# Performance work log

Hardware: AMD Instinct MI355X
Metric: run time of the kernel (lower is better)

## Reference

```python
import jax, jax.numpy as jnp
import numpy as np

HIDDEN = 1024
B, S = 4, 2048

def setup_inputs() -> dict:
    key = jax.random.key(0)
    ks = jax.random.split(key, 8)
    scale = 1.0 / np.sqrt(HIDDEN)
    return {
        "x": jax.random.normal(ks[0], (B, S, HIDDEN), dtype=jnp.float32),
        "mask": jax.random.randint(ks[1], (B, S, S), 0, 2, dtype=jnp.int32),
        "Wq": jax.random.normal(ks[2], (HIDDEN, HIDDEN), dtype=jnp.float32) * scale,
        "bq": jax.random.normal(ks[3], (HIDDEN,), dtype=jnp.float32) * 0.01,
        "Wk": jax.random.normal(ks[4], (HIDDEN, HIDDEN), dtype=jnp.float32) * scale,
        "bk": jax.random.normal(ks[5], (HIDDEN,), dtype=jnp.float32) * 0.01,
        "Wv": jax.random.normal(ks[6], (HIDDEN, HIDDEN), dtype=jnp.float32) * scale,
        "bv": jax.random.normal(ks[7], (HIDDEN,), dtype=jnp.float32) * 0.01,
    }

def reference(x, mask, Wq, bq, Wk, bk, Wv, bv):
    # torch Linear: y = x @ W.T + b
    Q = jnp.einsum("bsh,oh->bso", x, Wq) + bq
    K = jnp.einsum("bsh,oh->bso", x, Wk) + bk
    V = jnp.einsum("bsh,oh->bso", x, Wv) + bv
    inv_sqrt_h = 1.0 / jnp.sqrt(jnp.asarray(Q.shape[-1], Q.dtype))
    score = jnp.einsum("bqh,bkh->bqk", Q, K) * inv_sqrt_h  # [B, S, S]
    score = jnp.where(mask == 0, jnp.asarray(-jnp.inf, score.dtype), score)
    attn = jax.nn.softmax(score, axis=-1)
    return jnp.einsum("bqk,bkh->bqh", attn, V)
```

## Files before the change

### kernel.cpp

```cpp
#include <hip/hip_runtime.h>

using u16 = unsigned short;
using u32 = unsigned int;

typedef __attribute__((ext_vector_type(4))) float f32x4;
typedef __attribute__((ext_vector_type(8))) short s16x8;

__device__ __forceinline__ u16 f2b(float f) {
  u32 u = __builtin_bit_cast(u32, f);
  u += 0x7FFFu + ((u >> 16) & 1u);
  return (u16)(u >> 16);
}
__device__ __forceinline__ float b2f(u16 h) {
  return __builtin_bit_cast(float, (u32)h << 16);
}
__device__ __forceinline__ void gl_lds16(const void* g, void* l) {
  __builtin_amdgcn_global_load_lds(
      (const __attribute__((address_space(1))) void*)g,
      (__attribute__((address_space(3))) void*)l, 16, 0, 0);
}

__global__ __launch_bounds__(256) void convert4_k(
    const float* __restrict__ x, const float* __restrict__ Wq,
    const float* __restrict__ Wk, const float* __restrict__ Wv,
    u16* __restrict__ dst) {
  long g = (long)(blockIdx.x * 256 + threadIdx.x) * 8;
  const float* s;
  if (g < 8388608L)       s = x  + g;
  else if (g < 9437184L)  s = Wq + (g - 8388608L);
  else if (g < 10485760L) s = Wk + (g - 9437184L);
  else                    s = Wv + (g - 10485760L);
  f32x4 lo = *(const f32x4*)s;
  f32x4 hi = *(const f32x4*)(s + 4);
  s16x8 o;
  #pragma unroll
  for (int e = 0; e < 4; ++e) { o[e] = (short)f2b(lo[e]); o[4 + e] = (short)f2b(hi[e]); }
  *(s16x8*)(dst + g) = o;
}

template<int EPI>
__global__ __launch_bounds__(256) void gemm_bt(
    const u16* __restrict__ A, const u16* __restrict__ B0,
    const u16* __restrict__ W2, const u16* __restrict__ W3,
    int lda, int ldb, int K, long za, long zb, long ze,
    const float* __restrict__ bq, const float* __restrict__ bk, const float* __restrict__ bv,
    u16* __restrict__ qw, u16* __restrict__ kw, u16* __restrict__ vt,
    const int* __restrict__ mask, u16* __restrict__ sc, float* __restrict__ outO)
{
  __shared__ __align__(16) u16 lds[128 * 32 * 2];
  const int tid = threadIdx.x;
  const int wave = tid >> 6, lane = tid & 63;
  const int wr = wave >> 1, wc = wave & 1;
  const int m0 = blockIdx.y * 128, n0 = blockIdx.x * 128;
  const long z = blockIdx.z;
  A += z * za;

  const u16* Bsrc = B0;
  int nbase = n0;
  if constexpr (EPI == 0) {
    Bsrc = (n0 < 1024) ? B0 : (n0 < 2048) ? W2 : W3;
    nbase = n0 & 1023;
  }
  Bsrc += z * zb;

  u16* As = lds;
  u16* Bs = lds + 128 * 32;

  f32x4 acc[4][4];
  const f32x4 fz = {0.f, 0.f, 0.f, 0.f};
  #pragma unroll
  for (int i = 0; i < 4; ++i)
    #pragma unroll
    for (int j = 0; j < 4; ++j) acc[i][j] = fz;

  const int frow = lane & 15;
  const int q    = lane >> 4;

  for (int k0 = 0; k0 < K; k0 += 32) {
    __syncthreads();
    #pragma unroll
    for (int call = 0; call < 2; ++call) {
      int c = call * 256 + tid;
      int row = c >> 2;
      int kc = (c & 3) ^ (row & 3);
      const u16* ga = A    + (size_t)(m0    + row) * lda + (k0 + kc * 8);
      const u16* gb = Bsrc + (size_t)(nbase + row) * ldb + (k0 + kc * 8);
      u16* la = As + (size_t)(call * 256 + wave * 64) * 8;
      u16* lb = Bs + (size_t)(call * 256 + wave * 64) * 8;
      gl_lds16(ga, la);
      gl_lds16(gb, lb);
    }
    __syncthreads();

    s16x8 af[4], bf[4];
    #pragma unroll
    for (int i = 0; i < 4; ++i) {
      int lr = wr * 64 + i * 16 + frow;
      af[i] = *(const s16x8*)(As + lr * 32 + ((q ^ (lr & 3)) << 3));
    }
    #pragma unroll
    for (int j = 0; j < 4; ++j) {
      int lc = wc * 64 + j * 16 + frow;
      bf[j] = *(const s16x8*)(Bs + lc * 32 + ((q ^ (lc & 3)) << 3));
    }
    #pragma unroll
    for (int i = 0; i < 4; ++i)
      #pragma unroll
      for (int j = 0; j < 4; ++j)
        acc[i][j] = __builtin_amdgcn_mfma_f32_16x16x32_bf16(af[i], bf[j], acc[i][j], 0, 0, 0);
  }

  const int r0 = (lane >> 4) * 4;
  const int ccol = lane & 15;
  #pragma unroll
  for (int i = 0; i < 4; ++i) {
    #pragma unroll
    for (int j = 0; j < 4; ++j) {
      #pragma unroll
      for (int r = 0; r < 4; ++r) {
        int R = m0 + wr * 64 + i * 16 + r0 + r;
        int C = n0 + wc * 64 + j * 16 + ccol;
        float v = acc[i][j][r];
        if constexpr (EPI == 0) {
          int sec = C >> 10, nl = C & 1023;
          v += (sec == 0) ? bq[nl] : (sec == 1) ? bk[nl] : bv[nl];
          u16 o = f2b(v);
          int b = R >> 11, s = R & 2047;
          if (sec == 0)      qw[(size_t)R * 1024 + nl] = o;
          else if (sec == 1) kw[(size_t)R * 1024 + nl] = o;
          else               vt[(size_t)b * 2097152u + (size_t)nl * 2048 + s] = o;
        } else if constexpr (EPI == 1) {
          v *= 0.03125f;
          size_t idx = (size_t)(z * ze) + (size_t)R * 2048 + C;
          if (mask[idx] == 0) v = -__builtin_inff();
          sc[idx] = f2b(v);
        } else {
          outO[(size_t)(z * ze) + (size_t)R * 1024 + C] = v;
        }
      }
    }
  }
}

__global__ __launch_bounds__(256) void softmax_k(u16* __restrict__ Sc) {
  __shared__ float red[8];
  u16* p = Sc + (size_t)blockIdx.x * 2048;
  const int tid = threadIdx.x;
  const int lane = tid & 63, wv = tid >> 6;
  s16x8 u = *(const s16x8*)(p + tid * 8);
  float v[8];
  #pragma unroll
  for (int e = 0; e < 8; ++e) v[e] = b2f((u16)u[e]);
  float mx = v[0];
  #pragma unroll
  for (int e = 1; e < 8; ++e) mx = fmaxf(mx, v[e]);
  #pragma unroll
  for (int off = 32; off > 0; off >>= 1) mx = fmaxf(mx, __shfl_xor(mx, off));
  if (lane == 0) red[wv] = mx;
  __syncthreads();
  mx = fmaxf(fmaxf(red[0], red[1]), fmaxf(red[2], red[3]));
  float s = 0.f;
  #pragma unroll
  for (int e = 0; e < 8; ++e) { v[e] = __expf(v[e] - mx); s += v[e]; }
  #pragma unroll
  for (int off = 32; off > 0; off >>= 1) s += __shfl_xor(s, off);
  if (lane == 0) red[4 + wv] = s;
  __syncthreads();
  s = (red[4] + red[5]) + (red[6] + red[7]);
  float inv = 1.f / s;
  s16x8 o;
  #pragma unroll
  for (int e = 0; e < 8; ++e) o[e] = (short)f2b(v[e] * inv);
  *(s16x8*)(p + tid * 8) = o;
}

extern "C" void kernel_launch(void* const* d_in, const int* in_sizes, int n_in,
                              void* d_out, int out_size, void* d_ws, size_t ws_size,
                              hipStream_t stream) {
  const float* x  = (const float*)d_in[0];
  const int* mask = (const int*)d_in[1];
  const float* Wq = (const float*)d_in[2];
  const float* bq = (const float*)d_in[3];
  const float* Wk = (const float*)d_in[4];
  const float* bk = (const float*)d_in[5];
  const float* Wv = (const float*)d_in[6];
  const float* bv = (const float*)d_in[7];
  float* out = (float*)d_out;
  char* ws = (char*)d_ws;

  u16* xc  = (u16*)ws;
  u16* Wqc = (u16*)(ws + (16u << 20));
  u16* Wkc = (u16*)(ws + (18u << 20));
  u16* Wvc = (u16*)(ws + (20u << 20));
  u16* Qw  = (u16*)(ws + (22u << 20));
  u16* Kw  = (u16*)(ws + (38u << 20));
  u16* Vt  = (u16*)(ws + (54u << 20));
  u16* Sc  = (u16*)(ws + (70u << 20));

  convert4_k<<<5632, 256, 0, stream>>>(x, Wq, Wk, Wv, xc);

  gemm_bt<0><<<dim3(24, 64, 1), 256, 0, stream>>>(
      xc, Wqc, Wkc, Wvc, 1024, 1024, 1024, 0, 0, 0,
      bq, bk, bv, Qw, Kw, Vt, nullptr, nullptr, nullptr);
  gemm_bt<1><<<dim3(16, 16, 4), 256, 0, stream>>>(
      Qw, Kw, nullptr, nullptr, 1024, 1024, 1024, 2097152, 2097152, 4194304,
      nullptr, nullptr, nullptr, nullptr, nullptr, nullptr, mask, Sc, nullptr);
  softmax_k<<<8192, 256, 0, stream>>>(Sc);
  gemm_bt<2><<<dim3(8, 16, 4), 256, 0, stream>>>(
      Sc, Vt, nullptr, nullptr, 2048, 2048, 2048, 4194304, 2097152, 2097152,
      nullptr, nullptr, nullptr, nullptr, nullptr, nullptr, nullptr, nullptr, out);
}
```

Baseline: 371.0 us.

## Fuse softmax into QK and PV GEMM epilogues with bit-packed mask

Drops the standalone softmax kernel. The QK GEMM epilogue now computes exp(score) with no max subtraction, zeros masked entries using a mask packed to bits in the prep kernel, and accumulates per-row sums into a global buffer with atomics. The PV GEMM epilogue divides by that row sum. The aim is to avoid a full read and write of the score matrix and the strided int32 mask reads in the epilogue. The cost is extra mask-packing work, atomic contention, and possible exp overflow because the row max is no longer subtracted. The new path only runs when the workspace is at least 112 MB.

```diff
diff --git a/kernel.cpp b/kernel.cpp
--- a/kernel.cpp
+++ b/kernel.cpp
@@ -20,22 +20,43 @@
       (__attribute__((address_space(3))) void*)l, 16, 0, 0);
 }
 
-__global__ __launch_bounds__(256) void convert4_k(
+__global__ __launch_bounds__(256) void prep_k(
     const float* __restrict__ x, const float* __restrict__ Wq,
     const float* __restrict__ Wk, const float* __restrict__ Wv,
-    u16* __restrict__ dst) {
-  long g = (long)(blockIdx.x * 256 + threadIdx.x) * 8;
-  const float* s;
-  if (g < 8388608L)       s = x  + g;
-  else if (g < 9437184L)  s = Wq + (g - 8388608L);
-  else if (g < 10485760L) s = Wk + (g - 9437184L);
-  else                    s = Wv + (g - 10485760L);
-  f32x4 lo = *(const f32x4*)s;
-  f32x4 hi = *(const f32x4*)(s + 4);
-  s16x8 o;
-  #pragma unroll
-  for (int e = 0; e < 4; ++e) { o[e] = (short)f2b(lo[e]); o[4 + e] = (short)f2b(hi[e]); }
-  *(s16x8*)(dst + g) = o;
+    u16* __restrict__ dst, const int* __restrict__ mask,
+    u32* __restrict__ mb, float* __restrict__ Lrow) {
+  int blk = blockIdx.x;
+  if (blk < 5632) {
+    long g = (long)(blk * 256 + threadIdx.x) * 8;
+    const float* s;
+    if (g < 8388608L)       s = x  + g;
+    else if (g < 9437184L)  s = Wq + (g - 8388608L);
+    else if (g < 10485760L) s = Wk + (g - 9437184L);
+    else                    s = Wv + (g - 10485760L);
+    f32x4 lo = *(const f32x4*)s;
+    f32x4 hi = *(const f32x4*)(s + 4);
+    s16x8 o;
+    #pragma unroll
+    for (int e = 0; e < 4; ++e) { o[e] = (short)f2b(lo[e]); o[4 + e] = (short)f2b(hi[e]); }
+    *(s16x8*)(dst + g) = o;
+  } else if (blk < 7680) {
+    long t = (long)(blk - 5632) * 256 + threadIdx.x;
+    const int* mp = mask + t * 32;
+    u32 w = 0;
+    #pragma unroll
+    for (int c = 0; c < 8; ++c) {
+      int4 m4 = *(const int4*)(mp + c * 4);
+      w |= (u32)(m4.x != 0) << (c * 4);
+      w |= (u32)(m4.y != 0) << (c * 4 + 1);
+      w |= (u32)(m4.z != 0) << (c * 4 + 2);
+      w |= (u32)(m4.w != 0) << (c * 4 + 3);
+    }
+    mb[t] = w;
+  } else {
+    float* p = Lrow + threadIdx.x * 32;
+    #pragma unroll
+    for (int c = 0; c < 8; ++c) *(f32x4*)(p + c * 4) = (f32x4){0.f, 0.f, 0.f, 0.f};
+  }
 }
 
 template<int EPI>
@@ -45,7 +66,8 @@
     int lda, int ldb, int K, long za, long zb, long ze,
     const float* __restrict__ bq, const float* __restrict__ bk, const float* __restrict__ bv,
     u16* __restrict__ qw, u16* __restrict__ kw, u16* __restrict__ vt,
-    const int* __restrict__ mask, u16* __restrict__ sc, float* __restrict__ outO)
+    const int* __restrict__ mask, const u32* __restrict__ mbits,
+    float* __restrict__ Lrow, u16* __restrict__ sc, float* __restrict__ outO)
 {
   __shared__ __align__(16) u16 lds[128 * 32 * 2];
   const int tid = threadIdx.x;
@@ -112,16 +134,17 @@
 
   const int r0 = (lane >> 4) * 4;
   const int ccol = lane & 15;
-  #pragma unroll
-  for (int i = 0; i < 4; ++i) {
-    #pragma unroll
-    for (int j = 0; j < 4; ++j) {
-      #pragma unroll
-      for (int r = 0; r < 4; ++r) {
-        int R = m0 + wr * 64 + i * 16 + r0 + r;
-        int C = n0 + wc * 64 + j * 16 + ccol;
-        float v = acc[i][j][r];
-        if constexpr (EPI == 0) {
+
+  if constexpr (EPI == 0) {
+    #pragma unroll
+    for (int i = 0; i < 4; ++i) {
+      #pragma unroll
+      for (int j = 0; j < 4; ++j) {
+        #pragma unroll
+        for (int r = 0; r < 4; ++r) {
+          int R = m0 + wr * 64 + i * 16 + r0 + r;
+          int C = n0 + wc * 64 + j * 16 + ccol;
+          float v = acc[i][j][r];
           int sec = C >> 10, nl = C & 1023;
           v += (sec == 0) ? bq[nl] : (sec == 1) ? bk[nl] : bv[nl];
           u16 o = f2b(v);
@@ -129,13 +152,73 @@
           if (sec == 0)      qw[(size_t)R * 1024 + nl] = o;
           else if (sec == 1) kw[(size_t)R * 1024 + nl] = o;
           else               vt[(size_t)b * 2097152u + (size_t)nl * 2048 + s] = o;
-        } else if constexpr (EPI == 1) {
-          v *= 0.03125f;
-          size_t idx = (size_t)(z * ze) + (size_t)R * 2048 + C;
-          if (mask[idx] == 0) v = -__builtin_inff();
-          sc[idx] = f2b(v);
-        } else {
-          outO[(size_t)(z * ze) + (size_t)R * 1024 + C] = v;
+        }
+      }
+    }
+  } else if constexpr (EPI == 1) {
+    if (mbits) {
+      float rs[4][4];
+      #pragma unroll
+      for (int i = 0; i < 4; ++i)
+        #pragma unroll
+        for (int r = 0; r < 4; ++r) rs[i][r] = 0.f;
+      #pragma unroll
+      for (int i = 0; i < 4; ++i) {
+        #pragma unroll
+        for (int j = 0; j < 4; ++j) {
+          #pragma unroll
+          for (int r = 0; r < 4; ++r) {
+            int R = m0 + wr * 64 + i * 16 + r0 + r;
+            int C = n0 + wc * 64 + j * 16 + ccol;
+            float v = acc[i][j][r] * 0.03125f;
+            size_t idx = (size_t)(z * ze) + (size_t)R * 2048 + C;
+            u32 w = mbits[idx >> 5];
+            float e = ((w >> (idx & 31)) & 1u) ? __expf(v) : 0.f;
+            u16 eb = f2b(e);
+            sc[idx] = eb;
+            rs[i][r] += b2f(eb);
+          }
+        }
+      }
+      #pragma unroll
+      for (int i = 0; i < 4; ++i) {
+        #pragma unroll
+        for (int r = 0; r < 4; ++r) {
+          float s_ = rs[i][r];
+          s_ += __shfl_xor(s_, 1);
+          s_ += __shfl_xor(s_, 2);
+          s_ += __shfl_xor(s_, 4);
+          s_ += __shfl_xor(s_, 8);
+          if ((lane & 15) == 0)
+            atomicAdd(Lrow + z * 2048 + m0 + wr * 64 + i * 16 + r0 + r, s_);
+        }
+      }
+    } else {
+      #pragma unroll
+      for (int i = 0; i < 4; ++i)
+        #pragma unroll
+        for (int j = 0; j < 4; ++j)
+          #pragma unroll
+          for (int r = 0; r < 4; ++r) {
+            int R = m0 + wr * 64 + i * 16 + r0 + r;
+            int C = n0 + wc * 64 + j * 16 + ccol;
+            float v = acc[i][j][r] * 0.03125f;
+            size_t idx = (size_t)(z * ze) + (size_t)R * 2048 + C;
+            if (mask[idx] == 0) v = -__builtin_inff();
+            sc[idx] = f2b(v);
+          }
+    }
+  } else {
+    #pragma unroll
+    for (int i = 0; i < 4; ++i) {
+      #pragma unroll
+      for (int r = 0; r < 4; ++r) {
+        int R = m0 + wr * 64 + i * 16 + r0 + r;
+        float inv = Lrow ? (1.f / Lrow[z * 2048 + R]) : 1.f;
+        #pragma unroll
+        for (int j = 0; j < 4; ++j) {
+          int C = n0 + wc * 64 + j * 16 + ccol;
+          outO[(size_t)(z * ze) + (size_t)R * 1024 + C] = acc[i][j][r] * inv;
         }
       }
     }
@@ -188,25 +271,52 @@
   float* out = (float*)d_out;
   char* ws = (char*)d_ws;
 
-  u16* xc  = (u16*)ws;
-  u16* Wqc = (u16*)(ws + (16u << 20));
-  u16* Wkc = (u16*)(ws + (18u << 20));
-  u16* Wvc = (u16*)(ws + (20u << 20));
-  u16* Qw  = (u16*)(ws + (22u << 20));
-  u16* Kw  = (u16*)(ws + (38u << 20));
-  u16* Vt  = (u16*)(ws + (54u << 20));
-  u16* Sc  = (u16*)(ws + (70u << 20));
-
-  convert4_k<<<5632, 256, 0, stream>>>(x, Wq, Wk, Wv, xc);
-
-  gemm_bt<0><<<dim3(24, 64, 1), 256, 0, stream>>>(
-      xc, Wqc, Wkc, Wvc, 1024, 1024, 1024, 0, 0, 0,
-      bq, bk, bv, Qw, Kw, Vt, nullptr, nullptr, nullptr);
-  gemm_bt<1><<<dim3(16, 16, 4), 256, 0, stream>>>(
-      Qw, Kw, nullptr, nullptr, 1024, 1024, 1024, 2097152, 2097152, 4194304,
-      nullptr, nullptr, nullptr, nullptr, nullptr, nullptr, mask, Sc, nullptr);
-  softmax_k<<<8192, 256, 0, stream>>>(Sc);
-  gemm_bt<2><<<dim3(8, 16, 4), 256, 0, stream>>>(
-      Sc, Vt, nullptr, nullptr, 2048, 2048, 2048, 4194304, 2097152, 2097152,
-      nullptr, nullptr, nullptr, nullptr, nullptr, nullptr, nullptr, nullptr, out);
-}
+  if (ws_size >= (size_t)112 * 1024 * 1024) {
+    float* Lrow = (float*)ws;
+    u32* Mb  = (u32*)(ws + (1u << 20));
+    u16* xc  = (u16*)(ws + (4u << 20));
+    u16* Wqc = (u16*)(ws + (20u << 20));
+    u16* Wkc = (u16*)(ws + (22u << 20));
+    u16* Wvc = (u16*)(ws + (24u << 20));
+    u16* Qw  = (u16*)(ws + (26u << 20));
+    u16* Kw  = (u16*)(ws + (42u << 20));
+    u16* Vt  = (u16*)(ws + (58u << 20));
+    u16* Sc  = (u16*)(ws + (74u << 20));
+
+    prep_k<<<7681, 256, 0, stream>>>(x, Wq, Wk, Wv, xc, mask, Mb, Lrow);
+    gemm_bt<0><<<dim3(24, 64, 1), 256, 0, stream>>>(
+        xc, Wqc, Wkc, Wvc, 1024, 1024, 1024, 0, 0, 0,
+        bq, bk, bv, Qw, Kw, Vt, nullptr, nullptr, nullptr, nullptr, nullptr);
+    gemm_bt<1><<<dim3(16, 16, 4), 256, 0, stream>>>(
+        Qw, Kw, nullptr, nullptr, 1024, 1024, 1024, 2097152, 2097152, 4194304,
+        nullptr, nullptr, nullptr, nullptr, nullptr, nullptr,
+        nullptr, Mb, Lrow, Sc, nullptr);
+    gemm_bt<2><<<dim3(8, 16, 4), 256, 0, stream>>>(
+        Sc, Vt, nullptr, nullptr, 2048, 2048, 2048, 4194304, 2097152, 2097152,
+        nullptr, nullptr, nullptr, nullptr, nullptr, nullptr,
+        nullptr, nullptr, Lrow, nullptr, out);
+  } else {
+    u16* xc  = (u16*)ws;
+    u16* Wqc = (u16*)(ws + (16u << 20));
+    u16* Wkc = (u16*)(ws + (18u << 20));
+    u16* Wvc = (u16*)(ws + (20u << 20));
+    u16* Qw  = (u16*)(ws + (22u << 20));
+    u16* Kw  = (u16*)(ws + (38u << 20));
+    u16* Vt  = (u16*)(ws + (54u << 20));
+    u16* Sc  = (u16*)(ws + (70u << 20));
+
+    prep_k<<<5632, 256, 0, stream>>>(x, Wq, Wk, Wv, xc, mask, nullptr, nullptr);
+    gemm_bt<0><<<dim3(24, 64, 1), 256, 0, stream>>>(
+        xc, Wqc, Wkc, Wvc, 1024, 1024, 1024, 0, 0, 0,
+        bq, bk, bv, Qw, Kw, Vt, nullptr, nullptr, nullptr, nullptr, nullptr);
+    gemm_bt<1><<<dim3(16, 16, 4), 256, 0, stream>>>(
+        Qw, Kw, nullptr, nullptr, 1024, 1024, 1024, 2097152, 2097152, 4194304,
+        nullptr, nullptr, nullptr, nullptr, nullptr, nullptr,
+        mask, nullptr, nullptr, Sc, nullptr);
+    softmax_k<<<8192, 256, 0, stream>>>(Sc);
+    gemm_bt<2><<<dim3(8, 16, 4), 256, 0, stream>>>(
+        Sc, Vt, nullptr, nullptr, 2048, 2048, 2048, 4194304, 2097152, 2097152,
+        nullptr, nullptr, nullptr, nullptr, nullptr, nullptr,
+        nullptr, nullptr, nullptr, nullptr, out);
+  }
+}
```

New measurement: 390.8 us. 1.05x slower.
